# Performance work log

Measured on AMD Instinct MI355X. Metric: run time of the kernel, lower is better.

## Reference

```python
import jax, jax.numpy as jnp
import numpy as np

N, E = 50000, 800000
DIM_IN, DIM_H, DIM_OUT, HEADS = 128, 32, 16, 4
HID = DIM_H * HEADS  # 128
FINAL = DIM_OUT * HEADS  # 64
NEG_SLOPE = 0.2


def _glorot(key, shape):
    fan_in, fan_out = shape[0], shape[-1] if len(shape) > 1 else shape[0]
    lim = jnp.sqrt(6.0 / (fan_in + fan_out)).astype(jnp.float32)
    return jax.random.uniform(key, shape, jnp.float32, -lim, lim)


def setup_inputs() -> dict:
    key = jax.random.key(0)
    ks = jax.random.split(key, 16)
    x = jax.random.normal(ks[0], (N, DIM_IN), jnp.float32)
    edge_index = jax.random.randint(ks[1], (2, E), 0, N, dtype=jnp.int64)
    inp = {"x": x, "edge_index": edge_index}
    # layer 1: DIM_IN -> HEADS*DIM_H
    inp["Wl1"] = _glorot(ks[2], (DIM_IN, HEADS * DIM_H))
    inp["Wr1"] = _glorot(ks[3], (DIM_IN, HEADS * DIM_H))
    inp["att1"] = _glorot(ks[4], (HEADS, DIM_H))
    inp["b1"] = jnp.zeros((HEADS * DIM_H,), jnp.float32)
    # layer 2: HID -> HEADS*DIM_H
    inp["Wl2"] = _glorot(ks[5], (HID, HEADS * DIM_H))
    inp["Wr2"] = _glorot(ks[6], (HID, HEADS * DIM_H))
    inp["att2"] = _glorot(ks[7], (HEADS, DIM_H))
    inp["b2"] = jnp.zeros((HEADS * DIM_H,), jnp.float32)
    # layer 3: HID -> HEADS*DIM_OUT
    inp["Wl3"] = _glorot(ks[8], (HID, HEADS * DIM_OUT))
    inp["Wr3"] = _glorot(ks[9], (HID, HEADS * DIM_OUT))
    inp["att3"] = _glorot(ks[10], (HEADS, DIM_OUT))
    inp["b3"] = jnp.zeros((HEADS * DIM_OUT,), jnp.float32)
    return inp


def gatv2_conv(x, src, dst, Wl, Wr, att, b, heads, ch):
    n = x.shape[0]
    xl = (x @ Wl).reshape(n, heads, ch)  # source-side transform
    xr = (x @ Wr).reshape(n, heads, ch)  # target-side transform
    m = xl[src] + xr[dst]                 # [E, H, C]
    e = jnp.einsum('ehc,hc->eh', jax.nn.leaky_relu(m, NEG_SLOPE), att)
    # segment softmax over incoming edges of each dst node
    emax = jax.ops.segment_max(e, dst, num_segments=n)
    ex = jnp.exp(e - emax[dst])
    denom = jax.ops.segment_sum(ex, dst, num_segments=n)
    alpha = ex / denom[dst]               # [E, H]
    out = jax.ops.segment_sum(alpha[:, :, None] * xl[src], dst, num_segments=n)
    return out.reshape(n, heads * ch) + b


def reference(x, edge_index, Wl1, Wr1, att1, b1, Wl2, Wr2, att2, b2, Wl3, Wr3, att3, b3):
    n = x.shape[0]
    loops = jnp.arange(n, dtype=edge_index.dtype)
    src = jnp.concatenate([edge_index[0], loops])  # PyG add_self_loops=True
    dst = jnp.concatenate([edge_index[1], loops])
    # dropout is identity in eval mode
    h = jax.nn.elu(gatv2_conv(x, src, dst, Wl1, Wr1, att1, b1, HEADS, DIM_H))
    h = jax.nn.elu(gatv2_conv(h, src, dst, Wl2, Wr2, att2, b2, HEADS, DIM_H))
    h = gatv2_conv(h, src, dst, Wl3, Wr3, att3, b3, HEADS, DIM_OUT)
    return jax.nn.log_softmax(h, axis=1)
```

## Files before the change

### kernel.cpp

```cpp
#include <hip/hip_runtime.h>
#include <math.h>

constexpr int DIN  = 128;
constexpr int FSH  = 8;
constexpr int NFBM = 200;
constexpr int LCAP = 72;
constexpr int RND  = 4096;
constexpr int FCAP = 4608;

typedef __attribute__((ext_vector_type(8))) short short8;
typedef __attribute__((ext_vector_type(4))) float f32x4;

__device__ __forceinline__ unsigned short f2bf(float f) {
  unsigned u = __float_as_uint(f);
  u = (u + 0x7FFF + ((u >> 16) & 1)) >> 16;
  return (unsigned short)u;
}
__device__ __forceinline__ float bflo(unsigned u) { return __uint_as_float(u << 16); }
__device__ __forceinline__ float bfhi(unsigned u) { return __uint_as_float(u & 0xFFFF0000u); }

__device__ __forceinline__ void unpack8(uint4 u, float* x) {
  x[0] = bflo(u.x); x[1] = bfhi(u.x); x[2] = bflo(u.y); x[3] = bfhi(u.y);
  x[4] = bflo(u.z); x[5] = bfhi(u.z); x[6] = bflo(u.w); x[7] = bfhi(u.w);
}
__device__ __forceinline__ void unpack4(uint2 u, float* x) {
  x[0] = bflo(u.x); x[1] = bfhi(u.x); x[2] = bflo(u.y); x[3] = bfhi(u.y);
}

typedef const __attribute__((address_space(1))) unsigned int guint_t;
typedef __attribute__((address_space(3))) unsigned int luint_t;
__device__ __forceinline__ void async16(const void* g, void* l) {
  __builtin_amdgcn_global_load_lds((guint_t*)g, (luint_t*)l, 16, 0, 0);
}


__global__ __launch_bounds__(256) void prep_kernel(const int* __restrict__ ei,
    int* __restrict__ gcnt, unsigned* __restrict__ gpairs, int E, int nfb, int appb,
    const float* __restrict__ Wl1, const float* __restrict__ Wr1,
    const float* __restrict__ Wl2, const float* __restrict__ Wr2,
    const float* __restrict__ Wl3, const float* __restrict__ Wr3,
    unsigned short* __restrict__ Wt) {
  __shared__ unsigned buf[NFBM * LCAP];
  __shared__ int cnt[NFBM];
  __shared__ int gbase[NFBM];
  const int tid = threadIdx.x;

  if (blockIdx.x >= appb) {
    int e = (blockIdx.x - appb) * 256 + tid;
    if (e >= 81920) return;
    const float* src; int N; int off;
    if (e < 65536) {
      int m = e >> 14; off = e & 16383; N = 128;
      src = (m == 0) ? Wl1 : (m == 1) ? Wr1 : (m == 2) ? Wl2 : Wr2;
    } else {
      int e2 = e - 65536; int m = e2 >> 13; off = e2 & 8191; N = 64;
      src = m ? Wr3 : Wl3;
    }
    int nn = off >> 7, k = off & 127;
    Wt[e] = f2bf(src[(size_t)k * N + nn]);
    return;
  }

  if (tid < NFBM) cnt[tid] = 0;
  __syncthreads();

  const int k0 = blockIdx.x * RND;
  for (int i = tid; i < RND; i += 256) {
    int k = k0 + i;
    if (k >= E) break;
    int src = ei[k], dst = ei[E + k];
    int fb = dst >> FSH;
    int pos = atomicAdd(&cnt[fb], 1);
    if (pos < LCAP)
      buf[fb * LCAP + pos] = (unsigned)src | ((unsigned)(dst & ((1 << FSH) - 1)) << 16);
  }
  __syncthreads();

  if (tid < nfb) gbase[tid] = atomicAdd(&gcnt[tid], min(cnt[tid], LCAP));
  __syncthreads();

  const int wid = tid >> 6, lane = tid & 63;
  for (int fb = wid; fb < nfb; fb += 4) {
    int c  = min(cnt[fb], LCAP);
    int gb = gbase[fb];
    if (gb >= FCAP) continue;
    c = min(c, FCAP - gb);
    unsigned* dstp = gpairs + (size_t)fb * FCAP + gb;
    const unsigned* srcp = &buf[fb * LCAP];
    for (int i = lane; i < c; i += 64) dstp[i] = srcp[i];
  }
}


struct BuildSmem { int hist[1 << FSH]; int wsum[4]; int base_s; };

__device__ __forceinline__ void build_body(BuildSmem& s, int b,
    const unsigned* __restrict__ gpairs, const int* __restrict__ gcnt,
    int* __restrict__ row_ptr, unsigned short* __restrict__ edge_src,
    int n, int nfb) {
  const int tid = threadIdx.x;
  const int lane = tid & 63, wid = tid >> 6;

  const int d0 = b << FSH;
  const int nvalid = min(1 << FSH, n - d0);

  if (wid == 0) {
    int term = 0;
    for (int i = lane; i < b; i += 64)
      term += min(gcnt[i], FCAP) + min(1 << FSH, n - (i << FSH));
#pragma unroll
    for (int o = 32; o >= 1; o >>= 1) term += __shfl_xor(term, o, 64);
    if (lane == 0) s.base_s = term;
  }
  s.hist[tid] = (tid < nvalid) ? 1 : 0;
  __syncthreads();

  const int cnt = min(gcnt[b], FCAP);
  const unsigned* bp = gpairs + (size_t)b * FCAP;
  for (int i = tid; i < cnt; i += 256)
    atomicAdd(&s.hist[bp[i] >> 16], 1);
  __syncthreads();

  const int h = s.hist[tid];
  int incl = h;
#pragma unroll
  for (int o = 1; o < 64; o <<= 1) {
    int t = __shfl_up(incl, o, 64);
    if (lane >= o) incl += t;
  }
  if (lane == 63) s.wsum[wid] = incl;
  __syncthreads();
  int wo = 0;
  for (int wq = 0; wq < wid; ++wq) wo += s.wsum[wq];
  const int base = s.base_s;
  const int excl = wo + incl - h;
  if (tid < nvalid) {
    row_ptr[d0 + tid] = base + excl;
    edge_src[base + excl] = (unsigned short)(d0 + tid);
    s.hist[tid] = excl + 1;
  } else if (d0 + tid == n) {
    row_ptr[n] = base + excl;
  }
  if (b == nfb - 1 && d0 + (1 << FSH) <= n && tid == 0)
    row_ptr[n] = base + cnt + nvalid;
  __syncthreads();

  for (int i = tid; i < cnt; i += 256) {
    unsigned p = bp[i];
    int pos = atomicAdd(&s.hist[p >> 16], 1);
    edge_src[base + pos] = (unsigned short)(p & 0xFFFFu);
  }
}


template<int NC, bool CVT>
__device__ __forceinline__ void gemm2_body(char* lds, int bid, const void* __restrict__ Ap,
    const unsigned short* __restrict__ Wlt, const unsigned short* __restrict__ Wrt,
    unsigned short* __restrict__ outl, unsigned short* __restrict__ outr, int M) {
  constexpr int WNB = NC / 16;
  char* As = lds;
  char* Ws = lds + 16384;
  const int tid  = threadIdx.x;
  const int w    = tid >> 6, lane = tid & 63;
  const int q    = lane >> 4, r15 = lane & 15;
  const int row0 = bid * 64;

  if constexpr (CVT) {
    const float* Af = (const float*)Ap;
    for (int idx = tid * 4; idx < 64 * 128; idx += 1024) {
      int rl = idx >> 7, k = idx & 127;
      int rg = row0 + rl; if (rg >= M) rg = M - 1;
      float4 v = *(const float4*)&Af[(size_t)rg * 128 + k];
      uint2 pk;
      pk.x = (unsigned)f2bf(v.x) | ((unsigned)f2bf(v.y) << 16);
      pk.y = (unsigned)f2bf(v.z) | ((unsigned)f2bf(v.w) << 16);
      char* addr = As + (rl >> 4) * 4096 + (k >> 5) * 1024 +
                   ((((k >> 3) & 3) * 16) + (rl & 15)) * 16 + (k & 7) * 2;
      *(uint2*)addr = pk;
    }
  } else {
    const unsigned short* A = (const unsigned short*)Ap;
    int r = row0 + w * 16 + r15; if (r >= M) r = M - 1;
    const char* g = (const char*)A + (size_t)r * 256 + q * 16;
    char* l = As + w * 4096;
#pragma unroll
    for (int kk = 0; kk < 4; ++kk) async16(g + kk * 64, l + kk * 1024);
  }
  for (int nt = w; nt < WNB; nt += 4) {
    const char* g = (const char*)Wlt + ((size_t)(nt * 16 + r15)) * 256 + q * 16;
    char* l = Ws + nt * 4096;
#pragma unroll
    for (int kk = 0; kk < 4; ++kk) async16(g + kk * 64, l + kk * 1024);
  }
  __syncthreads();

  const char* aw = As + w * 4096;
  f32x4 acc[WNB] = {};
#pragma unroll
  for (int kk = 0; kk < 4; ++kk) {
    short8 af = *(const short8*)(aw + kk * 1024 + (size_t)lane * 16);
#pragma unroll
    for (int nt = 0; nt < WNB; ++nt) {
      short8 bf = *(const short8*)(Ws + (nt * 4 + kk) * 1024 + (size_t)lane * 16);
      acc[nt] = __builtin_amdgcn_mfma_f32_16x16x32_bf16(af, bf, acc[nt], 0, 0, 0);
    }
  }
  {
    int rowb = row0 + w * 16 + q * 4;
#pragma unroll
    for (int nt = 0; nt < WNB; ++nt)
#pragma unroll
      for (int r = 0; r < 4; ++r) {
        int rr = rowb + r;
        if (rr < M) outl[(size_t)rr * NC + nt * 16 + r15] = f2bf(acc[nt][r]);
      }
  }
  __syncthreads();
  for (int nt = w; nt < WNB; nt += 4) {
    const char* g = (const char*)Wrt + ((size_t)(nt * 16 + r15)) * 256 + q * 16;
    char* l = Ws + nt * 4096;
#pragma unroll
    for (int kk = 0; kk < 4; ++kk) async16(g + kk * 64, l + kk * 1024);
  }
  __syncthreads();

  f32x4 acc2[WNB] = {};
#pragma unroll
  for (int kk = 0; kk < 4; ++kk) {
    short8 af = *(const short8*)(aw + kk * 1024 + (size_t)lane * 16);
#pragma unroll
    for (int nt = 0; nt < WNB; ++nt) {
      short8 bf = *(const short8*)(Ws + (nt * 4 + kk) * 1024 + (size_t)lane * 16);
      acc2[nt] = __builtin_amdgcn_mfma_f32_16x16x32_bf16(af, bf, acc2[nt], 0, 0, 0);
    }
  }
  {
    int rowb = row0 + w * 16 + q * 4;
#pragma unroll
    for (int nt = 0; nt < WNB; ++nt)
#pragma unroll
      for (int r = 0; r < 4; ++r) {
        int rr = rowb + r;
        if (rr < M) outr[(size_t)rr * NC + nt * 16 + r15] = f2bf(acc2[nt][r]);
      }
  }
}

template<int NC, bool CVT>
__global__ __launch_bounds__(256) void gemm2_mfma(const void* __restrict__ Ap,
    const unsigned short* __restrict__ Wlt, const unsigned short* __restrict__ Wrt,
    unsigned short* __restrict__ outl, unsigned short* __restrict__ outr, int M) {
  __shared__ char lds[16384 + NC * 256];
  gemm2_body<NC, CVT>(lds, blockIdx.x, Ap, Wlt, Wrt, outl, outr, M);
}


union GemmBuildSmem { char lds[16384 + 128 * 256]; BuildSmem b; };

__global__ __launch_bounds__(256) void gemm1_build_kernel(const void* __restrict__ Ap,
    const unsigned short* __restrict__ Wlt, const unsigned short* __restrict__ Wrt,
    unsigned short* __restrict__ outl, unsigned short* __restrict__ outr,
    const unsigned* __restrict__ gpairs, const int* __restrict__ gcnt,
    int* __restrict__ row_ptr, unsigned short* __restrict__ edge_src,
    int n, int nfb) {
  __shared__ GemmBuildSmem smem;
  if (blockIdx.x < (unsigned)nfb)
    build_body(smem.b, blockIdx.x, gpairs, gcnt, row_ptr, edge_src, n, nfb);
  else
    gemm2_body<128, true>(smem.lds, blockIdx.x - nfb, Ap, Wlt, Wrt, outl, outr, n);
}


__global__ __launch_bounds__(256) void aggregate128_kernel(
    const unsigned short* __restrict__ xl, const unsigned short* __restrict__ xr,
    const float* __restrict__ att, const float* __restrict__ bias,
    const int* __restrict__ row_ptr, const unsigned short* __restrict__ edge_src,
    unsigned short* __restrict__ out, int n) {
  const int tid  = threadIdx.x;
  const int r    = tid & 15;
  const int node = blockIdx.x * 16 + (tid >> 4);
  if (node >= n) return;
  const int c0 = r * 8;

  float xrv[8];
  unpack8(*(const uint4*)&xr[(size_t)node * 128 + c0], xrv);
  float a6[8], a4[8];
  {
    float4 aa = *(const float4*)&att[c0];
    float4 ab = *(const float4*)&att[c0 + 4];
    float at[8] = {aa.x, aa.y, aa.z, aa.w, ab.x, ab.y, ab.z, ab.w};
#pragma unroll
    for (int j = 0; j < 8; ++j) { a6[j] = 0.6f * at[j]; a4[j] = 0.4f * at[j]; }
  }

  float l = 0.f, o[8] = {};
  int idx = row_ptr[node];
  const int end = row_ptr[node + 1];

  int s0 = 0, s1 = 0, s2 = 0, s3 = 0;
  if (idx + 4 <= end) {
    s0 = edge_src[idx];     s1 = edge_src[idx + 1];
    s2 = edge_src[idx + 2]; s3 = edge_src[idx + 3];
  }
  while (idx + 4 <= end) {
    uint4 u0 = *(const uint4*)&xl[(size_t)s0 * 128 + c0];
    uint4 u1 = *(const uint4*)&xl[(size_t)s1 * 128 + c0];
    uint4 u2 = *(const uint4*)&xl[(size_t)s2 * 128 + c0];
    uint4 u3 = *(const uint4*)&xl[(size_t)s3 * 128 + c0];
    idx += 4;
    if (idx + 4 <= end) {
      s0 = edge_src[idx];     s1 = edge_src[idx + 1];
      s2 = edge_src[idx + 2]; s3 = edge_src[idx + 3];
    }
    float x0[8], x1[8], x2[8], x3[8];
    unpack8(u0, x0); unpack8(u1, x1); unpack8(u2, x2); unpack8(u3, x3);
    float p0 = 0.f, p1 = 0.f, p2 = 0.f, p3 = 0.f;
#pragma unroll
    for (int j = 0; j < 8; ++j) {
      float t0 = x0[j] + xrv[j], t1 = x1[j] + xrv[j];
      float t2 = x2[j] + xrv[j], t3 = x3[j] + xrv[j];
      p0 = fmaf(t0, a6[j], p0); p0 = fmaf(fabsf(t0), a4[j], p0);
      p1 = fmaf(t1, a6[j], p1); p1 = fmaf(fabsf(t1), a4[j], p1);
      p2 = fmaf(t2, a6[j], p2); p2 = fmaf(fabsf(t2), a4[j], p2);
      p3 = fmaf(t3, a6[j], p3); p3 = fmaf(fabsf(t3), a4[j], p3);
    }
    p0 += __shfl_xor(p0, 1, 64); p0 += __shfl_xor(p0, 2, 64);
    p1 += __shfl_xor(p1, 1, 64); p1 += __shfl_xor(p1, 2, 64);
    p2 += __shfl_xor(p2, 1, 64); p2 += __shfl_xor(p2, 2, 64);
    p3 += __shfl_xor(p3, 1, 64); p3 += __shfl_xor(p3, 2, 64);
    float e0 = __expf(fminf(p0, 80.f)), e1 = __expf(fminf(p1, 80.f));
    float e2 = __expf(fminf(p2, 80.f)), e3 = __expf(fminf(p3, 80.f));
    l += (e0 + e1) + (e2 + e3);
#pragma unroll
    for (int j = 0; j < 8; ++j)
      o[j] = fmaf(e0, x0[j], fmaf(e1, x1[j], fmaf(e2, x2[j], fmaf(e3, x3[j], o[j]))));
  }
  for (; idx < end; ++idx) {
    int s = edge_src[idx];
    uint4 u0 = *(const uint4*)&xl[(size_t)s * 128 + c0];
    float x0[8];
    unpack8(u0, x0);
    float p0 = 0.f;
#pragma unroll
    for (int j = 0; j < 8; ++j) {
      float t = x0[j] + xrv[j];
      p0 = fmaf(t, a6[j], p0); p0 = fmaf(fabsf(t), a4[j], p0);
    }
    p0 += __shfl_xor(p0, 1, 64); p0 += __shfl_xor(p0, 2, 64);
    float e0 = __expf(fminf(p0, 80.f));
    l += e0;
#pragma unroll
    for (int j = 0; j < 8; ++j) o[j] = fmaf(e0, x0[j], o[j]);
  }

  float4 b0 = *(const float4*)&bias[c0];
  float4 b1 = *(const float4*)&bias[c0 + 4];
  float bb[8] = {b0.x, b0.y, b0.z, b0.w, b1.x, b1.y, b1.z, b1.w};
  float rl = 1.f / l;
  unsigned short res[8];
#pragma unroll
  for (int j = 0; j < 8; ++j) {
    float v = o[j] * rl + bb[j];
    v = v > 0.f ? v : __expf(v) - 1.f;
    res[j] = f2bf(v);
  }
  uint4 ov;
  ov.x = (unsigned)res[0] | ((unsigned)res[1] << 16);
  ov.y = (unsigned)res[2] | ((unsigned)res[3] << 16);
  ov.z = (unsigned)res[4] | ((unsigned)res[5] << 16);
  ov.w = (unsigned)res[6] | ((unsigned)res[7] << 16);
  *(uint4*)&out[(size_t)node * 128 + c0] = ov;
}


__global__ __launch_bounds__(256) void aggregate64_kernel(
    const unsigned short* __restrict__ xl, const unsigned short* __restrict__ xr,
    const float* __restrict__ att, const float* __restrict__ bias,
    const int* __restrict__ row_ptr, const unsigned short* __restrict__ edge_src,
    float* __restrict__ out, int n) {
  const int tid  = threadIdx.x;
  const int r    = tid & 15;
  const int node = blockIdx.x * 16 + (tid >> 4);
  if (node >= n) return;
  const int c0 = r * 4;

  float xrv[4];
  unpack4(*(const uint2*)&xr[(size_t)node * 64 + c0], xrv);
  float a6[4], a4[4];
  {
    float4 aa = *(const float4*)&att[c0];
    float at[4] = {aa.x, aa.y, aa.z, aa.w};
#pragma unroll
    for (int j = 0; j < 4; ++j) { a6[j] = 0.6f * at[j]; a4[j] = 0.4f * at[j]; }
  }

  float l = 0.f, o[4] = {};
  int idx = row_ptr[node];
  const int end = row_ptr[node + 1];

  int s0 = 0, s1 = 0, s2 = 0, s3 = 0;
  if (idx + 4 <= end) {
    s0 = edge_src[idx];     s1 = edge_src[idx + 1];
    s2 = edge_src[idx + 2]; s3 = edge_src[idx + 3];
  }
  while (idx + 4 <= end) {
    uint2 u0 = *(const uint2*)&xl[(size_t)s0 * 64 + c0];
    uint2 u1 = *(const uint2*)&xl[(size_t)s1 * 64 + c0];
    uint2 u2 = *(const uint2*)&xl[(size_t)s2 * 64 + c0];
    uint2 u3 = *(const uint2*)&xl[(size_t)s3 * 64 + c0];
    idx += 4;
    if (idx + 4 <= end) {
      s0 = edge_src[idx];     s1 = edge_src[idx + 1];
      s2 = edge_src[idx + 2]; s3 = edge_src[idx + 3];
    }
    float x0[4], x1[4], x2[4], x3[4];
    unpack4(u0, x0); unpack4(u1, x1); unpack4(u2, x2); unpack4(u3, x3);
    float p0 = 0.f, p1 = 0.f, p2 = 0.f, p3 = 0.f;
#pragma unroll
    for (int j = 0; j < 4; ++j) {
      float t0 = x0[j] + xrv[j], t1 = x1[j] + xrv[j];
      float t2 = x2[j] + xrv[j], t3 = x3[j] + xrv[j];
      p0 = fmaf(t0, a6[j], p0); p0 = fmaf(fabsf(t0), a4[j], p0);
      p1 = fmaf(t1, a6[j], p1); p1 = fmaf(fabsf(t1), a4[j], p1);
      p2 = fmaf(t2, a6[j], p2); p2 = fmaf(fabsf(t2), a4[j], p2);
      p3 = fmaf(t3, a6[j], p3); p3 = fmaf(fabsf(t3), a4[j], p3);
    }
    p0 += __shfl_xor(p0, 1, 64); p0 += __shfl_xor(p0, 2, 64);
    p1 += __shfl_xor(p1, 1, 64); p1 += __shfl_xor(p1, 2, 64);
    p2 += __shfl_xor(p2, 1, 64); p2 += __shfl_xor(p2, 2, 64);
    p3 += __shfl_xor(p3, 1, 64); p3 += __shfl_xor(p3, 2, 64);
    float e0 = __expf(fminf(p0, 80.f)), e1 = __expf(fminf(p1, 80.f));
    float e2 = __expf(fminf(p2, 80.f)), e3 = __expf(fminf(p3, 80.f));
    l += (e0 + e1) + (e2 + e3);
#pragma unroll
    for (int j = 0; j < 4; ++j)
      o[j] = fmaf(e0, x0[j], fmaf(e1, x1[j], fmaf(e2, x2[j], fmaf(e3, x3[j], o[j]))));
  }
  for (; idx < end; ++idx) {
    int s = edge_src[idx];
    uint2 u0 = *(const uint2*)&xl[(size_t)s * 64 + c0];
    float x0[4];
    unpack4(u0, x0);
    float p0 = 0.f;
#pragma unroll
    for (int j = 0; j < 4; ++j) {
      float t = x0[j] + xrv[j];
      p0 = fmaf(t, a6[j], p0); p0 = fmaf(fabsf(t), a4[j], p0);
    }
    p0 += __shfl_xor(p0, 1, 64); p0 += __shfl_xor(p0, 2, 64);
    float e0 = __expf(fminf(p0, 80.f));
    l += e0;
#pragma unroll
    for (int j = 0; j < 4; ++j) o[j] = fmaf(e0, x0[j], o[j]);
  }

  float4 bv = *(const float4*)&bias[c0];
  float bb[4] = {bv.x, bv.y, bv.z, bv.w};
  float rl = 1.f / l;
  float rr[4];
#pragma unroll
  for (int j = 0; j < 4; ++j) rr[j] = o[j] * rl + bb[j];

  float mx = fmaxf(fmaxf(rr[0], rr[1]), fmaxf(rr[2], rr[3]));
#pragma unroll
  for (int off = 1; off < 16; off <<= 1) mx = fmaxf(mx, __shfl_xor(mx, off, 64));
  float se = __expf(rr[0] - mx) + __expf(rr[1] - mx) +
             __expf(rr[2] - mx) + __expf(rr[3] - mx);
#pragma unroll
  for (int off = 1; off < 16; off <<= 1) se += __shfl_xor(se, off, 64);
  float ls = mx + __logf(se);
  *(float4*)&out[(size_t)node * 64 + c0] =
      make_float4(rr[0] - ls, rr[1] - ls, rr[2] - ls, rr[3] - ls);
}


extern "C" void kernel_launch(void* const* d_in, const int* in_sizes, int n_in,
                              void* d_out, int out_size, void* d_ws, size_t ws_size,
                              hipStream_t stream) {
  const float* x    = (const float*)d_in[0];
  const int*   ei   = (const int*)d_in[1];
  const float* Wl1  = (const float*)d_in[2];
  const float* Wr1  = (const float*)d_in[3];
  const float* att1 = (const float*)d_in[4];
  const float* b1   = (const float*)d_in[5];
  const float* Wl2  = (const float*)d_in[6];
  const float* Wr2  = (const float*)d_in[7];
  const float* att2 = (const float*)d_in[8];
  const float* b2   = (const float*)d_in[9];
  const float* Wl3  = (const float*)d_in[10];
  const float* Wr3  = (const float*)d_in[11];
  const float* att3 = (const float*)d_in[12];
  const float* b3   = (const float*)d_in[13];
  const int n = in_sizes[0] / DIN;
  const int E = in_sizes[1] / 2;
  float* out = (float*)d_out;

  const int nfb  = (n + (1 << FSH) - 1) >> FSH;
  const int appb = (E + RND - 1) / RND;

  unsigned short* xl = (unsigned short*)d_ws;
  unsigned short* xr = xl + (size_t)n * 128;
  unsigned short* h  = xr + (size_t)n * 128;
  unsigned short* Wt = h + (size_t)n * 128;
  unsigned short* Wl1t = Wt, *Wr1t = Wt + 16384;
  unsigned short* Wl2t = Wt + 32768, *Wr2t = Wt + 49152;
  unsigned short* Wl3t = Wt + 65536, *Wr3t = Wt + 73728;
  int* row_ptr  = (int*)(Wt + 81920);
  int* gcnt     = row_ptr + (n + 16);
  unsigned short* edge_src = (unsigned short*)(gcnt + NFBM);
  unsigned* gpairs = (unsigned*)((char*)edge_src +
      ((((size_t)(E + n) * 2) + 15) & ~(size_t)15));

  hipMemsetAsync(gcnt, 0, NFBM * sizeof(int), stream);

  prep_kernel<<<appb + 320, 256, 0, stream>>>(ei, gcnt, gpairs, E, nfb, appb,
                                              Wl1, Wr1, Wl2, Wr2, Wl3, Wr3, Wt);

  const int gb = (n + 63) / 64;
  const int ab = (n + 15) / 16;

  gemm1_build_kernel<<<nfb + gb, 256, 0, stream>>>(x, Wl1t, Wr1t, xl, xr,
                                                   gpairs, gcnt, row_ptr, edge_src, n, nfb);

  aggregate128_kernel<<<ab, 256, 0, stream>>>(xl, xr, att1, b1, row_ptr, edge_src, h, n);
  gemm2_mfma<128, false><<<gb, 256, 0, stream>>>(h, Wl2t, Wr2t, xl, xr, n);
  aggregate128_kernel<<<ab, 256, 0, stream>>>(xl, xr, att2, b2, row_ptr, edge_src, h, n);
  gemm2_mfma<64, false><<<gb, 256, 0, stream>>>(h, Wl3t, Wr3t, xl, xr, n);
  aggregate64_kernel<<<ab, 256, 0, stream>>>(xl, xr, att3, b3, row_ptr, edge_src, out, n);
}
```

Measured before the change: 265.5 us.

## Fuse GAT aggregation with next layer's dual MFMA projection in one kernel

Replaces the separate aggregate128 and gemm2 launches for layers 1→2 and 2→3 with a single 512-thread kernel. Each block first aggregates 64 destination nodes and writes the bf16 results directly into an LDS A-tile, then runs the Wl/Wr MFMA projections from LDS. Both weight matrices are prefetched asynchronously while the aggregation runs. This removes the global write and re-read of the hidden activations and two kernel launches. In exchange the blocks are larger and use more LDS, which can lower occupancy for the latency-bound edge gather, and xr is overwritten in place, relying on each block reading only its own rows.

```diff
diff --git a/kernel.cpp b/kernel.cpp
--- a/kernel.cpp
+++ b/kernel.cpp
@@ -246,14 +246,6 @@
   }
 }
 
-template<int NC, bool CVT>
-__global__ __launch_bounds__(256) void gemm2_mfma(const void* __restrict__ Ap,
-    const unsigned short* __restrict__ Wlt, const unsigned short* __restrict__ Wrt,
-    unsigned short* __restrict__ outl, unsigned short* __restrict__ outr, int M) {
-  __shared__ char lds[16384 + NC * 256];
-  gemm2_body<NC, CVT>(lds, blockIdx.x, Ap, Wlt, Wrt, outl, outr, M);
-}
-
 
 union GemmBuildSmem { char lds[16384 + 128 * 256]; BuildSmem b; };
 
@@ -271,17 +263,11 @@
 }
 
 
-__global__ __launch_bounds__(256) void aggregate128_kernel(
-    const unsigned short* __restrict__ xl, const unsigned short* __restrict__ xr,
+__device__ __forceinline__ uint4 agg128_node(
+    const unsigned short* __restrict__ xl, const unsigned short* xr,
     const float* __restrict__ att, const float* __restrict__ bias,
     const int* __restrict__ row_ptr, const unsigned short* __restrict__ edge_src,
-    unsigned short* __restrict__ out, int n) {
-  const int tid  = threadIdx.x;
-  const int r    = tid & 15;
-  const int node = blockIdx.x * 16 + (tid >> 4);
-  if (node >= n) return;
-  const int c0 = r * 8;
-
+    int node, int c0) {
   float xrv[8];
   unpack8(*(const uint4*)&xr[(size_t)node * 128 + c0], xrv);
   float a6[8], a4[8];
@@ -369,7 +355,78 @@
   ov.y = (unsigned)res[2] | ((unsigned)res[3] << 16);
   ov.z = (unsigned)res[4] | ((unsigned)res[5] << 16);
   ov.w = (unsigned)res[6] | ((unsigned)res[7] << 16);
-  *(uint4*)&out[(size_t)node * 128 + c0] = ov;
+  return ov;
+}
+
+
+template<int NC>
+__global__ __launch_bounds__(512, 4) void agg_gemm_kernel(
+    const unsigned short* __restrict__ xg,
+    const unsigned short* xr,
+    const float* __restrict__ att, const float* __restrict__ bias,
+    const int* __restrict__ row_ptr, const unsigned short* __restrict__ edge_src,
+    const unsigned short* __restrict__ Wlt, const unsigned short* __restrict__ Wrt,
+    unsigned short* outl, unsigned short* outr, int n) {
+  constexpr int WNB = NC / 16;
+  __shared__ char lds[16384 + 2 * NC * 256];
+  char* As  = lds;
+  char* WsL = lds + 16384;
+  char* WsR = WsL + NC * 256;
+  const int tid  = threadIdx.x;
+  const int w8   = tid >> 6, lane = tid & 63;
+  const int q    = lane >> 4, r15 = lane & 15;
+  const int row0 = blockIdx.x * 64;
+
+  {
+    const unsigned short* Wsrc = (w8 < 4) ? Wlt : Wrt;
+    char* Wdst = (w8 < 4) ? WsL : WsR;
+    const int wq = w8 & 3;
+    for (int nt = wq; nt < WNB; nt += 4) {
+      const char* g = (const char*)Wsrc + ((size_t)(nt * 16 + r15)) * 256 + q * 16;
+      char* l = Wdst + nt * 4096;
+#pragma unroll
+      for (int kk = 0; kk < 4; ++kk) async16(g + kk * 64, l + kk * 1024);
+    }
+  }
+
+  const int r   = tid & 15;
+  const int g16 = tid >> 4;
+  const int c0  = r * 8;
+#pragma unroll
+  for (int pass = 0; pass < 2; ++pass) {
+    const int rl   = pass * 32 + g16;
+    const int node = row0 + rl;
+    uint4 ov = make_uint4(0, 0, 0, 0);
+    if (node < n)
+      ov = agg128_node(xg, xr, att, bias, row_ptr, edge_src, node, c0);
+    char* addr = As + (rl >> 4) * 4096 + (r >> 2) * 1024 +
+                 (((r & 3) * 16) + (rl & 15)) * 16;
+    *(uint4*)addr = ov;
+  }
+  __syncthreads();
+
+  const char* Wsme = (w8 < 4) ? WsL : WsR;
+  unsigned short* outme = (w8 < 4) ? outl : outr;
+  const int wq = w8 & 3;
+  const char* aw = As + wq * 4096;
+  f32x4 acc[WNB] = {};
+#pragma unroll
+  for (int kk = 0; kk < 4; ++kk) {
+    short8 af = *(const short8*)(aw + kk * 1024 + (size_t)lane * 16);
+#pragma unroll
+    for (int nt = 0; nt < WNB; ++nt) {
+      short8 bf = *(const short8*)(Wsme + (nt * 4 + kk) * 1024 + (size_t)lane * 16);
+      acc[nt] = __builtin_amdgcn_mfma_f32_16x16x32_bf16(af, bf, acc[nt], 0, 0, 0);
+    }
+  }
+  const int rowb = row0 + wq * 16 + q * 4;
+#pragma unroll
+  for (int nt = 0; nt < WNB; ++nt)
+#pragma unroll
+    for (int rr4 = 0; rr4 < 4; ++rr4) {
+      int rr = rowb + rr4;
+      if (rr < n) outme[(size_t)rr * NC + nt * 16 + r15] = f2bf(acc[nt][rr4]);
+    }
 }
 
 
@@ -522,9 +579,12 @@
   gemm1_build_kernel<<<nfb + gb, 256, 0, stream>>>(x, Wl1t, Wr1t, xl, xr,
                                                    gpairs, gcnt, row_ptr, edge_src, n, nfb);
 
-  aggregate128_kernel<<<ab, 256, 0, stream>>>(xl, xr, att1, b1, row_ptr, edge_src, h, n);
-  gemm2_mfma<128, false><<<gb, 256, 0, stream>>>(h, Wl2t, Wr2t, xl, xr, n);
-  aggregate128_kernel<<<ab, 256, 0, stream>>>(xl, xr, att2, b2, row_ptr, edge_src, h, n);
-  gemm2_mfma<64, false><<<gb, 256, 0, stream>>>(h, Wl3t, Wr3t, xl, xr, n);
-  aggregate64_kernel<<<ab, 256, 0, stream>>>(xl, xr, att3, b3, row_ptr, edge_src, out, n);
-}
+  agg_gemm_kernel<128><<<gb, 512, 0, stream>>>(xl, xr, att1, b1, row_ptr, edge_src,
+                                               Wl2t, Wr2t, h, xr, n);
+
+  agg_gemm_kernel<64><<<gb, 512, 0, stream>>>(h, xr, att2, b2, row_ptr, edge_src,
+                                              Wl3t, Wr3t, xl, xl + (size_t)n * 64, n);
+
+  aggregate64_kernel<<<ab, 256, 0, stream>>>(xl, xl + (size_t)n * 64, att3, b3,
+                                             row_ptr, edge_src, out, n);
+}
```

New measurement: 261.3 us. No clear change (-1.6%).
